# Kernel optimization log

Hardware: AMD Instinct MI355X
Metric: run time of the kernel (lower is better)

Reference implementation:

```python
import jax, jax.numpy as jnp
import numpy as np

HEAD_DIM = 64
NUM_FEATURES = 256


def _sample_orf(head_dim, num_features, seed=0):
    """Orthogonal random features with chi(d)-norm row scaling (FAVOR+)."""
    rng = np.random.RandomState(seed)
    blocks = []
    while len(blocks) * head_dim < num_features:
        G = rng.randn(head_dim, head_dim).astype(np.float32)
        Q, _ = np.linalg.qr(G)
        norms = np.linalg.norm(rng.randn(head_dim, head_dim).astype(np.float32), axis=1)
        blocks.append(np.diag(norms) @ Q.T)
    return np.concatenate(blocks, axis=0)[:num_features].astype(np.float32)


def _phi(x, omega, is_query):
    """FAVOR+ positive feature map with max-subtraction stabilization."""
    m = omega.shape[0]
    proj = jnp.einsum('bhnd,md->bhnm', x, omega)          # [B,H,N,M]
    norm = 0.5 * jnp.sum(x * x, axis=-1, keepdims=True)    # [B,H,N,1]
    log_phi = proj - norm
    if is_query:
        log_phi = log_phi - jnp.max(log_phi, axis=-1, keepdims=True)
    else:
        log_phi = log_phi - jnp.max(log_phi)
    return jnp.exp(log_phi) / np.float32(np.sqrt(m)) + 1e-4


def _causal_scan(phi_q, phi_k, v):
    """Causal linear-attention recurrence via lax.scan. States: S[B,H,M,D], z[B,H,M]."""
    B, H, N, M = phi_q.shape
    D = v.shape[-1]
    # seq-first for scan: [N,B,H,*]
    pq = jnp.moveaxis(phi_q, 2, 0)
    pk = jnp.moveaxis(phi_k, 2, 0)
    vt = jnp.moveaxis(v, 2, 0)

    S0 = jnp.zeros((B, H, M, D), dtype=phi_q.dtype)
    z0 = jnp.zeros((B, H, M), dtype=phi_q.dtype)

    def step(carry, xs):
        S, z = carry
        pq_i, pk_i, v_i = xs  # [B,H,M], [B,H,M], [B,H,D]
        S = S + pk_i[..., :, None] * v_i[..., None, :]
        z = z + pk_i
        num = jnp.einsum('bhm,bhmd->bhd', pq_i, S)
        den = jnp.sum(pq_i * z, axis=-1, keepdims=True) + 1e-6
        return (S, z), num / den

    _, out = jax.lax.scan(step, (S0, z0), (pq, pk, vt))  # out: [N,B,H,D]
    return jnp.moveaxis(out, 0, 2)


def setup_inputs() -> dict:
    key = jax.random.key(0)
    k1, k2, k3 = jax.random.split(key, 3)
    B, H, N, D = 2, 16, 4096, HEAD_DIM
    q = jax.random.normal(k1, (B, H, N, D), dtype=jnp.float32)
    k = jax.random.normal(k2, (B, H, N, D), dtype=jnp.float32)
    v = jax.random.normal(k3, (B, H, N, D), dtype=jnp.float32)
    omega = jnp.asarray(_sample_orf(HEAD_DIM, NUM_FEATURES))
    return {"q": q, "k": k, "v": v, "omega": omega}


def reference(q, k, v, omega):
    scale = q.shape[-1] ** (-0.25)
    phi_q = _phi(q * scale, omega, is_query=True)
    phi_k = _phi(k * scale, omega, is_query=False)
    # q_len == kv_len -> causal scan branch (matches original forward)
    out = _causal_scan(phi_q.astype(jnp.float32), phi_k.astype(jnp.float32),
                       v.astype(jnp.float32))
    return out.astype(q.dtype)
```

## Files before the change

### kernel.cpp

```cpp
#include <hip/hip_runtime.h>
#include <cstddef>

#define BH    32
#define NSEQ  4096
#define MFEAT 256
#define CHUNK 128
#define NCH   32
#define SROW  65
#define SPITCH (SROW*256)

#define SCALE 0.35355339059327373f

typedef unsigned int uint_t;
typedef _Float16 half_t;
typedef __attribute__((ext_vector_type(8))) _Float16 half8;
typedef __attribute__((ext_vector_type(4))) float f32x4;

__device__ __forceinline__ f32x4 mfma16(half8 a, half8 b, f32x4 c) {
  return __builtin_amdgcn_mfma_f32_16x16x32_f16(a, b, c, 0, 0, 0);
}
__device__ __forceinline__ uint_t enc_f(float x) {
  uint_t u = __float_as_uint(x);
  return (u & 0x80000000u) ? ~u : (u | 0x80000000u);
}
__device__ __forceinline__ float dec_f(uint_t u) {
  u = (u & 0x80000000u) ? (u ^ 0x80000000u) : ~u;
  return __uint_as_float(u);
}
__device__ __forceinline__ half8 cvt_h8(float4 a, float4 b) {
  half8 h;
  h[0] = (half_t)a.x; h[1] = (half_t)a.y; h[2] = (half_t)a.z; h[3] = (half_t)a.w;
  h[4] = (half_t)b.x; h[5] = (half_t)b.y; h[6] = (half_t)b.z; h[7] = (half_t)b.w;
  return h;
}

__global__ void k_init(uint_t* kmax) { *kmax = enc_f(-__builtin_inff()); }

__global__ __launch_bounds__(256, 4) void k_maxes2(
    const float* __restrict__ q, const float* __restrict__ kx,
    const float* __restrict__ omega, float* __restrict__ rowmQ,
    uint_t* __restrict__ kmax, half_t* __restrict__ qh,
    half_t* __restrict__ kh, float* __restrict__ hnKg)
{
  __shared__ half_t Wl[256 * 72];
  __shared__ float nrm[64];
  __shared__ float red[4];

  const int tid = threadIdx.x;
  const int lane = tid & 63;
  const int w = tid >> 6;
  const int lc = lane & 15, rg = lane >> 4, koff = rg * 8;
  const size_t rowbase = (size_t)blockIdx.x * 64;

  for (int l = tid; l < 4096; l += 256) {
    int m = l >> 4, d4 = (l & 15) * 4;
    float4 o = *(const float4*)(omega + m * 64 + d4);
    half_t* p = &Wl[m * 72 + d4];
    p[0] = (half_t)o.x; p[1] = (half_t)o.y; p[2] = (half_t)o.z; p[3] = (half_t)o.w;
  }
  half8 aq[2], akf[2];
  {
    const float* qp = q + (rowbase + w * 16 + lc) * 64 + koff;
    const float* kp = kx + (rowbase + w * 16 + lc) * 64 + koff;
    float pn = 0.f;
    #pragma unroll
    for (int ks = 0; ks < 2; ks++) {
      float4 a = *(const float4*)(qp + ks * 32);
      float4 b = *(const float4*)(qp + ks * 32 + 4);
      a.x *= SCALE; a.y *= SCALE; a.z *= SCALE; a.w *= SCALE;
      b.x *= SCALE; b.y *= SCALE; b.z *= SCALE; b.w *= SCALE;
      aq[ks] = cvt_h8(a, b);
      float4 c = *(const float4*)(kp + ks * 32);
      float4 d = *(const float4*)(kp + ks * 32 + 4);
      c.x *= SCALE; c.y *= SCALE; c.z *= SCALE; c.w *= SCALE;
      d.x *= SCALE; d.y *= SCALE; d.z *= SCALE; d.w *= SCALE;
      pn += c.x * c.x + c.y * c.y + c.z * c.z + c.w * c.w
          + d.x * d.x + d.y * d.y + d.z * d.z + d.w * d.w;
      akf[ks] = cvt_h8(c, d);
    }
    #pragma unroll
    for (int ks = 0; ks < 2; ks++) {
      *(half8*)(qh + (rowbase + w * 16 + lc) * 64 + ks * 32 + koff) = aq[ks];
      *(half8*)(kh + (rowbase + w * 16 + lc) * 64 + ks * 32 + koff) = akf[ks];
    }
    pn += __shfl_xor(pn, 16, 64);
    pn += __shfl_xor(pn, 32, 64);
    if (rg == 0) {
      nrm[w * 16 + lc] = 0.5f * pn;
      hnKg[rowbase + w * 16 + lc] = 0.5f * pn;
    }
  }
  __syncthreads();

  float mrow[4] = {-3.4e38f, -3.4e38f, -3.4e38f, -3.4e38f};
  #pragma unroll
  for (int hh = 0; hh < 2; hh++) {
    f32x4 acc[8];
    #pragma unroll
    for (int c = 0; c < 8; c++) acc[c] = (f32x4){0.f, 0.f, 0.f, 0.f};
    #pragma unroll
    for (int ks = 0; ks < 2; ks++)
      #pragma unroll
      for (int c = 0; c < 8; c++) {
        half8 b = *(const half8*)&Wl[((hh * 8 + c) * 16 + lc) * 72 + ks * 32 + koff];
        acc[c] = mfma16(aq[ks], b, acc[c]);
      }
    #pragma unroll
    for (int c = 0; c < 8; c++)
      #pragma unroll
      for (int r = 0; r < 4; r++) mrow[r] = fmaxf(mrow[r], acc[c][r]);
  }
  #pragma unroll
  for (int r = 0; r < 4; r++) {
    float m0 = mrow[r];
    m0 = fmaxf(m0, __shfl_xor(m0, 1, 64));
    m0 = fmaxf(m0, __shfl_xor(m0, 2, 64));
    m0 = fmaxf(m0, __shfl_xor(m0, 4, 64));
    m0 = fmaxf(m0, __shfl_xor(m0, 8, 64));
    if (lc == 0) rowmQ[rowbase + w * 16 + rg * 4 + r] = m0;
  }

  float hn[4];
  #pragma unroll
  for (int r = 0; r < 4; r++) hn[r] = nrm[w * 16 + rg * 4 + r];
  float bm = -3.4e38f;
  #pragma unroll
  for (int hh = 0; hh < 2; hh++) {
    f32x4 acc[8];
    #pragma unroll
    for (int c = 0; c < 8; c++) acc[c] = (f32x4){0.f, 0.f, 0.f, 0.f};
    #pragma unroll
    for (int ks = 0; ks < 2; ks++)
      #pragma unroll
      for (int c = 0; c < 8; c++) {
        half8 b = *(const half8*)&Wl[((hh * 8 + c) * 16 + lc) * 72 + ks * 32 + koff];
        acc[c] = mfma16(akf[ks], b, acc[c]);
      }
    #pragma unroll
    for (int c = 0; c < 8; c++)
      #pragma unroll
      for (int r = 0; r < 4; r++) bm = fmaxf(bm, acc[c][r] - hn[r]);
  }
  #pragma unroll
  for (int off = 1; off < 64; off <<= 1) bm = fmaxf(bm, __shfl_xor(bm, off, 64));
  if (lane == 0) red[w] = bm;
  __syncthreads();
  if (tid == 0)
    atomicMax(kmax, enc_f(fmaxf(fmaxf(red[0], red[1]), fmaxf(red[2], red[3]))));
}

__global__ __launch_bounds__(256, 2) void k_state2(
    const half_t* __restrict__ kh, const float* __restrict__ v,
    const float* __restrict__ omega, const float* __restrict__ hnKg,
    const uint_t* __restrict__ kmax, half_t* __restrict__ spA)
{
  __shared__ half_t WP[256 * 72];
  __shared__ half_t vt[80 * 136];

  const int tid = threadIdx.x;
  const int lane = tid & 63;
  const int w = tid >> 6;
  const int lc = lane & 15, rg = lane >> 4, koff = rg * 8;
  const int wr = w * 32;
  const int blk = blockIdx.x;
  const size_t nbase = (size_t)(blk >> 5) * NSEQ + (size_t)(blk & 31) * CHUNK;
  const float gmaxv = dec_f(*kmax);

  for (int l = tid; l < 4096; l += 256) {
    int m = l >> 4, d4 = (l & 15) * 4;
    float4 o = *(const float4*)(omega + m * 64 + d4);
    half_t* p = &WP[m * 72 + d4];
    p[0] = (half_t)o.x; p[1] = (half_t)o.y; p[2] = (half_t)o.z; p[3] = (half_t)o.w;
  }
  for (int l = tid; l < 2048; l += 256) {
    int j = l >> 4, dq = (l & 15) * 4;
    float4 vv = *(const float4*)(v + (nbase + j) * 64 + dq);
    vt[(dq + 0) * 136 + j] = (half_t)vv.x;
    vt[(dq + 1) * 136 + j] = (half_t)vv.y;
    vt[(dq + 2) * 136 + j] = (half_t)vv.z;
    vt[(dq + 3) * 136 + j] = (half_t)vv.w;
  }
  if (tid < 128) vt[64 * 136 + tid] = (half_t)1.0f;

  half8 ak[2][2];
  float hnr[2][4];
  #pragma unroll
  for (int rt = 0; rt < 2; rt++) {
    const half_t* kp = kh + (nbase + wr + rt * 16 + lc) * 64 + koff;
    ak[rt][0] = *(const half8*)(kp);
    ak[rt][1] = *(const half8*)(kp + 32);
    #pragma unroll
    for (int r = 0; r < 4; r++)
      hnr[rt][r] = hnKg[nbase + wr + rt * 16 + rg * 4 + r];
  }
  __syncthreads();

  f32x4 accP[2][16];
  #pragma unroll
  for (int rt = 0; rt < 2; rt++)
    #pragma unroll
    for (int ct = 0; ct < 16; ct++) accP[rt][ct] = (f32x4){0.f, 0.f, 0.f, 0.f};
  #pragma unroll
  for (int ks = 0; ks < 2; ks++)
    #pragma unroll
    for (int ct = 0; ct < 16; ct++) {
      half8 b = *(const half8*)&WP[(ct * 16 + lc) * 72 + ks * 32 + koff];
      accP[0][ct] = mfma16(ak[0][ks], b, accP[0][ct]);
      accP[1][ct] = mfma16(ak[1][ks], b, accP[1][ct]);
    }
  #pragma unroll
  for (int rt = 0; rt < 2; rt++)
    #pragma unroll
    for (int ct = 0; ct < 16; ct++)
      #pragma unroll
      for (int r = 0; r < 4; r++)
        accP[rt][ct][r] = __expf(accP[rt][ct][r] - hnr[rt][r] - gmaxv) * 0.0625f + 1e-4f;

  half_t* pkT = WP;
  #pragma unroll
  for (int h = 0; h < 2; h++) {
    __syncthreads();
    #pragma unroll
    for (int rt = 0; rt < 2; rt++)
      #pragma unroll
      for (int c8 = 0; c8 < 8; c8++) {
        int ct = h * 8 + c8;
        #pragma unroll
        for (int r = 0; r < 4; r++)
          pkT[(c8 * 16 + lc) * 144 + wr + rt * 16 + rg * 4 + r] = (half_t)accP[rt][ct][r];
      }
    __syncthreads();
    f32x4 acc2[5][2];
    #pragma unroll
    for (int rt = 0; rt < 5; rt++) {
      acc2[rt][0] = (f32x4){0.f, 0.f, 0.f, 0.f};
      acc2[rt][1] = (f32x4){0.f, 0.f, 0.f, 0.f};
    }
    #pragma unroll
    for (int ks = 0; ks < 4; ks++) {
      half8 b0 = *(const half8*)&pkT[((2 * w + 0) * 16 + lc) * 144 + ks * 32 + koff];
      half8 b1 = *(const half8*)&pkT[((2 * w + 1) * 16 + lc) * 144 + ks * 32 + koff];
      #pragma unroll
      for (int rt = 0; rt < 5; rt++) {
        half8 a = *(const half8*)&vt[(rt * 16 + lc) * 136 + ks * 32 + koff];
        acc2[rt][0] = mfma16(a, b0, acc2[rt][0]);
        acc2[rt][1] = mfma16(a, b1, acc2[rt][1]);
      }
    }
    #pragma unroll
    for (int rt = 0; rt < 5; rt++)
      #pragma unroll
      for (int c2 = 0; c2 < 2; c2++)
        #pragma unroll
        for (int r = 0; r < 4; r++) {
          int row = rt * 16 + rg * 4 + r;
          if (row < SROW)
            spA[(size_t)blk * SPITCH + row * 256 + h * 128 + (2 * w + c2) * 16 + lc] =
                (half_t)acc2[rt][c2][r];
        }
  }
}

__global__ __launch_bounds__(256) void k_prefix(
    const uint_t* __restrict__ spA, uint_t* __restrict__ spB)
{
  int r = blockIdx.x * 256 + threadIdx.x;
  if (r >= SPITCH / 2) return;
  int bh = blockIdx.y;
  const uint_t* src = spA + (size_t)bh * NCH * (SPITCH / 2) + r;
  uint_t* dst = spB + (size_t)bh * NCH * (SPITCH / 2) + r;
  float r0 = 0.f, r1 = 0.f;
  for (int c = 0; c < NCH; c++) {
    union { uint_t u; half_t h[2]; } cv, ov;
    cv.u = src[(size_t)c * (SPITCH / 2)];
    ov.h[0] = (half_t)r0; ov.h[1] = (half_t)r1;
    dst[(size_t)c * (SPITCH / 2)] = ov.u;
    r0 += (float)cv.h[0];
    r1 += (float)cv.h[1];
  }
}

__global__ __launch_bounds__(256, 2) void k_attn7(
    const half_t* __restrict__ qh, const half_t* __restrict__ kh,
    const float* __restrict__ v, const float* __restrict__ omega,
    const float* __restrict__ rowmQ, const float* __restrict__ hnKg,
    const uint_t* __restrict__ kmax, const half_t* __restrict__ spB,
    float* __restrict__ out)
{
  __shared__ half_t sm[21504];
  half_t* PQ  = sm;
  half_t* PK  = sm + 8192;
  half_t* SST = sm + 16384;
  half_t* AS  = sm;
  half_t* VT  = sm + 8192;

  const int tid = threadIdx.x;
  const int lane = tid & 63;
  const int w = tid >> 6;
  const int lc = lane & 15, rg = lane >> 4, koff = rg * 8;
  const int wr = w * 32;
  const int blk = blockIdx.x;
  const size_t nbase = (size_t)(blk >> 5) * NSEQ + (size_t)(blk & 31) * CHUNK;
  const half_t* spb = spB + (size_t)blk * SPITCH;
  const float gmaxv = dec_f(*kmax);
  const int swz = (lc & 7) << 3;

  float rowm[2][4], hnr[2][4];
  #pragma unroll
  for (int rt = 0; rt < 2; rt++)
    #pragma unroll
    for (int r = 0; r < 4; r++) {
      rowm[rt][r] = rowmQ[nbase + wr + rt * 16 + rg * 4 + r];
      hnr[rt][r]  = hnKg[nbase + wr + rt * 16 + rg * 4 + r];
    }
  half8 aq[2][2], ak[2][2];
  #pragma unroll
  for (int rt = 0; rt < 2; rt++) {
    const half_t* qp = qh + (nbase + wr + rt * 16 + lc) * 64 + koff;
    const half_t* kp = kh + (nbase + wr + rt * 16 + lc) * 64 + koff;
    aq[rt][0] = *(const half8*)(qp);
    aq[rt][1] = *(const half8*)(qp + 32);
    ak[rt][0] = *(const half8*)(kp);
    ak[rt][1] = *(const half8*)(kp + 32);
  }

#define STAGEPHASE(MT) do {                                                   \
    { int ro = tid >> 3, c8 = (tid & 7) * 8;                                  \
      *(half8*)&SST[ro * 64 + (c8 ^ ((ro & 7) << 3))] =                       \
          *(const half8*)(spb + ro * 256 + (MT) * 64 + c8); }                 \
    { int l = tid + 256; int ro = l >> 3, c8 = (l & 7) * 8;                   \
      *(half8*)&SST[ro * 64 + (c8 ^ ((ro & 7) << 3))] =                       \
          *(const half8*)(spb + ro * 256 + (MT) * 64 + c8); }                 \
    if (tid < 8) { int l = tid + 512; int ro = l >> 3, c8 = (l & 7) * 8;      \
      *(half8*)&SST[ro * 64 + (c8 ^ ((ro & 7) << 3))] =                       \
          *(const half8*)(spb + ro * 256 + (MT) * 64 + c8); }                 \
    half8 bwl[4][2];                                                          \
    _Pragma("unroll") for (int ct = 0; ct < 4; ct++) {                        \
      const float* op = omega + ((MT) * 64 + ct * 16 + lc) * 64 + koff;       \
      bwl[ct][0] = cvt_h8(*(const float4*)(op), *(const float4*)(op + 4));    \
      bwl[ct][1] = cvt_h8(*(const float4*)(op + 32),                          \
                          *(const float4*)(op + 36));                         \
    }                                                                         \
    f32x4 accP[2][4];                                                         \
    _Pragma("unroll") for (int rt = 0; rt < 2; rt++)                          \
      _Pragma("unroll") for (int ct = 0; ct < 4; ct++)                        \
        accP[rt][ct] = (f32x4){0.f, 0.f, 0.f, 0.f};                           \
    _Pragma("unroll") for (int ks = 0; ks < 2; ks++)                          \
      _Pragma("unroll") for (int ct = 0; ct < 4; ct++) {                      \
        accP[0][ct] = mfma16(aq[0][ks], bwl[ct][ks], accP[0][ct]);            \
        accP[1][ct] = mfma16(aq[1][ks], bwl[ct][ks], accP[1][ct]);            \
      }                                                                       \
    _Pragma("unroll") for (int rt = 0; rt < 2; rt++)                          \
      _Pragma("unroll") for (int ct = 0; ct < 4; ct++)                        \
        _Pragma("unroll") for (int r = 0; r < 4; r++) {                       \
          int i = wr + rt * 16 + rg * 4 + r;                                  \
          float val = __expf(accP[rt][ct][r] - rowm[rt][r]) * 0.0625f + 1e-4f;\
          PQ[i * 64 + ((ct * 16 + lc) ^ ((i & 7) << 3))] = (half_t)val;       \
        }                                                                     \
    _Pragma("unroll") for (int rt = 0; rt < 2; rt++)                          \
      _Pragma("unroll") for (int ct = 0; ct < 4; ct++)                        \
        accP[rt][ct] = (f32x4){0.f, 0.f, 0.f, 0.f};                           \
    _Pragma("unroll") for (int ks = 0; ks < 2; ks++)                          \
      _Pragma("unroll") for (int ct = 0; ct < 4; ct++) {                      \
        accP[0][ct] = mfma16(ak[0][ks], bwl[ct][ks], accP[0][ct]);            \
        accP[1][ct] = mfma16(ak[1][ks], bwl[ct][ks], accP[1][ct]);            \
      }                                                                       \
    _Pragma("unroll") for (int rt = 0; rt < 2; rt++)                          \
      _Pragma("unroll") for (int ct = 0; ct < 4; ct++)                        \
        _Pragma("unroll") for (int r = 0; r < 4; r++) {                       \
          int i = wr + rt * 16 + rg * 4 + r;                                  \
          float val = __expf(accP[rt][ct][r] - hnr[rt][r] - gmaxv) * 0.0625f + 1e-4f; \
          PK[i * 64 + ((ct * 16 + lc) ^ ((i & 7) << 3))] = (half_t)val;       \
        }                                                                     \
  } while (0)

#define COMPUTEPHASE() do {                                                   \
    _Pragma("unroll") for (int ks2 = 0; ks2 < 64; ks2 += 32) {                \
      int sA = (ks2 + koff) ^ swz;                                            \
      half8 a0 = *(const half8*)&PQ[(wr + lc) * 64 + sA];                     \
      half8 a1 = *(const half8*)&PQ[(wr + 16 + lc) * 64 + sA];                \
      _Pragma("unroll") for (int ct = 0; ct < 8; ct++) {                      \
        half8 b = *(const half8*)&PK[(ct * 16 + lc) * 64 + sA];               \
        accA[0][ct] = mfma16(a0, b, accA[0][ct]);                             \
        accA[1][ct] = mfma16(a1, b, accA[1][ct]);                             \
      }                                                                       \
      _Pragma("unroll") for (int cs = 0; cs < 5; cs++) {                      \
        half8 b = *(const half8*)&SST[(cs * 16 + lc) * 64 + sA];              \
        accO[0][cs] = mfma16(a0, b, accO[0][cs]);                             \
        accO[1][cs] = mfma16(a1, b, accO[1][cs]);                             \
      }                                                                       \
    } } while (0)

  f32x4 accA[2][8], accO[2][5];
  #pragma unroll
  for (int rt = 0; rt < 2; rt++) {
    #pragma unroll
    for (int ct = 0; ct < 8; ct++) accA[rt][ct] = (f32x4){0.f, 0.f, 0.f, 0.f};
    #pragma unroll
    for (int cs = 0; cs < 5; cs++) accO[rt][cs] = (f32x4){0.f, 0.f, 0.f, 0.f};
  }

  for (int mt = 0; mt < 4; mt++) {
    STAGEPHASE(mt);
    __syncthreads();
    COMPUTEPHASE();
    __syncthreads();
  }

  for (int l = tid; l < 2048; l += 256) {
    int j = l >> 4, dq = (l & 15) * 4;
    float4 vv = *(const float4*)(v + (nbase + j) * 64 + dq);
    VT[(dq + 0) * 128 + (j ^ (((dq + 0) & 7) << 3))] = (half_t)vv.x;
    VT[(dq + 1) * 128 + (j ^ (((dq + 1) & 7) << 3))] = (half_t)vv.y;
    VT[(dq + 2) * 128 + (j ^ (((dq + 2) & 7) << 3))] = (half_t)vv.z;
    VT[(dq + 3) * 128 + (j ^ (((dq + 3) & 7) << 3))] = (half_t)vv.w;
  }
  if (tid < 128) VT[64 * 128 + tid] = (half_t)1.0f;

  #pragma unroll
  for (int h = 0; h < 2; h++) {
    #pragma unroll
    for (int rt = 0; rt < 2; rt++)
      #pragma unroll
      for (int c4 = 0; c4 < 4; c4++) {
        int ct = h * 4 + c4;
        int j = ct * 16 + lc;
        #pragma unroll
        for (int r = 0; r < 4; r++) {
          int i = wr + rt * 16 + rg * 4 + r;
          float val = (j <= i) ? accA[rt][ct][r] : 0.f;
          AS[i * 64 + ((j - h * 64) ^ ((i & 7) << 3))] = (half_t)val;
        }
      }
    if (h == 0) __syncthreads();
    #pragma unroll
    for (int ks2 = 0; ks2 < 64; ks2 += 32) {
      int sA = (ks2 + koff) ^ swz;
      int sV = (h * 64 + ks2 + koff) ^ swz;
      half8 a0 = *(const half8*)&AS[(wr + lc) * 64 + sA];
      half8 a1 = *(const half8*)&AS[(wr + 16 + lc) * 64 + sA];
      #pragma unroll
      for (int cs = 0; cs < 5; cs++) {
        half8 b = *(const half8*)&VT[(cs * 16 + lc) * 128 + sV];
        accO[0][cs] = mfma16(a0, b, accO[0][cs]);
        accO[1][cs] = mfma16(a1, b, accO[1][cs]);
      }
    }
  }

  #pragma unroll
  for (int rt = 0; rt < 2; rt++)
    #pragma unroll
    for (int r = 0; r < 4; r++) {
      float den = __shfl(accO[rt][4][r], (lane & 48), 64) + 1e-6f;
      float inv = 1.0f / den;
      int i = wr + rt * 16 + rg * 4 + r;
      #pragma unroll
      for (int cs = 0; cs < 4; cs++)
        out[(nbase + i) * 64 + cs * 16 + lc] = accO[rt][cs][r] * inv;
    }
#undef STAGEPHASE
#undef COMPUTEPHASE
}

extern "C" void kernel_launch(void* const* d_in, const int* in_sizes, int n_in,
                              void* d_out, int out_size, void* d_ws, size_t ws_size,
                              hipStream_t stream) {
  const float* q = (const float*)d_in[0];
  const float* k = (const float*)d_in[1];
  const float* v = (const float*)d_in[2];
  const float* omega = (const float*)d_in[3];
  float* out = (float*)d_out;
  char* ws = (char*)d_ws;

  float*  rowmQ = (float*)(ws + 0);
  float*  hnKg  = (float*)(ws + 524288);
  half_t* qh    = (half_t*)(ws + 1048576);
  half_t* kh    = (half_t*)(ws + 17825792);
  half_t* spA   = (half_t*)(ws + 34603008);
  half_t* spB   = (half_t*)(ws + 68681728);
  uint_t* kmax  = (uint_t*)(ws + 102760448);

  k_init<<<1, 1, 0, stream>>>(kmax);
  k_maxes2<<<2048, 256, 0, stream>>>(q, k, omega, rowmQ, kmax, qh, kh, hnKg);
  k_state2<<<1024, 256, 0, stream>>>(kh, v, omega, hnKg, kmax, spA);
  k_prefix<<<dim3(33, 32), 256, 0, stream>>>((const uint_t*)spA, (uint_t*)spB);
  k_attn7<<<1024, 256, 0, stream>>>(qh, kh, v, omega, rowmQ, hnKg, kmax, spB, out);
}
```

Measured before the change: 162.2 us.

## Materialize phiQ and phiK in earlier kernels instead of recomputing in attention

```diff
diff --git a/kernel.cpp b/kernel.cpp
--- a/kernel.cpp
+++ b/kernel.cpp
@@ -36,11 +36,11 @@
 
 __global__ void k_init(uint_t* kmax) { *kmax = enc_f(-__builtin_inff()); }
 
-__global__ __launch_bounds__(256, 4) void k_maxes2(
+__global__ __launch_bounds__(256, 2) void k_maxes3(
     const float* __restrict__ q, const float* __restrict__ kx,
-    const float* __restrict__ omega, float* __restrict__ rowmQ,
-    uint_t* __restrict__ kmax, half_t* __restrict__ qh,
-    half_t* __restrict__ kh, float* __restrict__ hnKg)
+    const float* __restrict__ omega, uint_t* __restrict__ kmax,
+    half_t* __restrict__ phiQ, half_t* __restrict__ kh,
+    float* __restrict__ hnKg)
 {
   __shared__ half_t Wl[256 * 72];
   __shared__ float nrm[64];
@@ -79,10 +79,8 @@
       akf[ks] = cvt_h8(c, d);
     }
     #pragma unroll
-    for (int ks = 0; ks < 2; ks++) {
-      *(half8*)(qh + (rowbase + w * 16 + lc) * 64 + ks * 32 + koff) = aq[ks];
+    for (int ks = 0; ks < 2; ks++)
       *(half8*)(kh + (rowbase + w * 16 + lc) * 64 + ks * 32 + koff) = akf[ks];
-    }
     pn += __shfl_xor(pn, 16, 64);
     pn += __shfl_xor(pn, 32, 64);
     if (rg == 0) {
@@ -92,67 +90,82 @@
   }
   __syncthreads();
 
-  float mrow[4] = {-3.4e38f, -3.4e38f, -3.4e38f, -3.4e38f};
-  #pragma unroll
-  for (int hh = 0; hh < 2; hh++) {
-    f32x4 acc[8];
-    #pragma unroll
-    for (int c = 0; c < 8; c++) acc[c] = (f32x4){0.f, 0.f, 0.f, 0.f};
+  {
+    f32x4 acc[16];
+    #pragma unroll
+    for (int ct = 0; ct < 16; ct++) acc[ct] = (f32x4){0.f, 0.f, 0.f, 0.f};
     #pragma unroll
     for (int ks = 0; ks < 2; ks++)
       #pragma unroll
-      for (int c = 0; c < 8; c++) {
-        half8 b = *(const half8*)&Wl[((hh * 8 + c) * 16 + lc) * 72 + ks * 32 + koff];
-        acc[c] = mfma16(aq[ks], b, acc[c]);
-      }
-    #pragma unroll
-    for (int c = 0; c < 8; c++)
-      #pragma unroll
-      for (int r = 0; r < 4; r++) mrow[r] = fmaxf(mrow[r], acc[c][r]);
-  }
+      for (int ct = 0; ct < 16; ct++) {
+        half8 b = *(const half8*)&Wl[(ct * 16 + lc) * 72 + ks * 32 + koff];
+        acc[ct] = mfma16(akf[ks], b, acc[ct]);
+      }
+    float hn[4];
+    #pragma unroll
+    for (int r = 0; r < 4; r++) hn[r] = nrm[w * 16 + rg * 4 + r];
+    float bm = -3.4e38f;
+    #pragma unroll
+    for (int ct = 0; ct < 16; ct++)
+      #pragma unroll
+      for (int r = 0; r < 4; r++) bm = fmaxf(bm, acc[ct][r] - hn[r]);
+    #pragma unroll
+    for (int off = 1; off < 64; off <<= 1) bm = fmaxf(bm, __shfl_xor(bm, off, 64));
+    if (lane == 0) red[w] = bm;
+  }
+
+  f32x4 acc[16];
+  #pragma unroll
+  for (int ct = 0; ct < 16; ct++) acc[ct] = (f32x4){0.f, 0.f, 0.f, 0.f};
+  #pragma unroll
+  for (int ks = 0; ks < 2; ks++)
+    #pragma unroll
+    for (int ct = 0; ct < 16; ct++) {
+      half8 b = *(const half8*)&Wl[(ct * 16 + lc) * 72 + ks * 32 + koff];
+      acc[ct] = mfma16(aq[ks], b, acc[ct]);
+    }
+  float rowm[4];
   #pragma unroll
   for (int r = 0; r < 4; r++) {
-    float m0 = mrow[r];
+    float m0 = -3.4e38f;
+    #pragma unroll
+    for (int ct = 0; ct < 16; ct++) m0 = fmaxf(m0, acc[ct][r]);
     m0 = fmaxf(m0, __shfl_xor(m0, 1, 64));
     m0 = fmaxf(m0, __shfl_xor(m0, 2, 64));
     m0 = fmaxf(m0, __shfl_xor(m0, 4, 64));
     m0 = fmaxf(m0, __shfl_xor(m0, 8, 64));
-    if (lc == 0) rowmQ[rowbase + w * 16 + rg * 4 + r] = m0;
-  }
-
-  float hn[4];
-  #pragma unroll
-  for (int r = 0; r < 4; r++) hn[r] = nrm[w * 16 + rg * 4 + r];
-  float bm = -3.4e38f;
-  #pragma unroll
-  for (int hh = 0; hh < 2; hh++) {
-    f32x4 acc[8];
-    #pragma unroll
-    for (int c = 0; c < 8; c++) acc[c] = (f32x4){0.f, 0.f, 0.f, 0.f};
-    #pragma unroll
-    for (int ks = 0; ks < 2; ks++)
-      #pragma unroll
-      for (int c = 0; c < 8; c++) {
-        half8 b = *(const half8*)&Wl[((hh * 8 + c) * 16 + lc) * 72 + ks * 32 + koff];
-        acc[c] = mfma16(akf[ks], b, acc[c]);
-      }
-    #pragma unroll
-    for (int c = 0; c < 8; c++)
-      #pragma unroll
-      for (int r = 0; r < 4; r++) bm = fmaxf(bm, acc[c][r] - hn[r]);
-  }
-  #pragma unroll
-  for (int off = 1; off < 64; off <<= 1) bm = fmaxf(bm, __shfl_xor(bm, off, 64));
-  if (lane == 0) red[w] = bm;
+    rowm[r] = m0;
+  }
+  #pragma unroll
+  for (int ct = 0; ct < 16; ct++)
+    #pragma unroll
+    for (int r = 0; r < 4; r++)
+      acc[ct][r] = __expf(acc[ct][r] - rowm[r]) * 0.0625f + 1e-4f;
+
   __syncthreads();
   if (tid == 0)
     atomicMax(kmax, enc_f(fmaxf(fmaxf(red[0], red[1]), fmaxf(red[2], red[3]))));
-}
-
-__global__ __launch_bounds__(256, 2) void k_state2(
+
+  half_t* st = Wl;
+  #pragma unroll
+  for (int ct = 0; ct < 16; ct++)
+    #pragma unroll
+    for (int r = 0; r < 4; r++)
+      st[(w * 16 + rg * 4 + r) * 264 + ct * 16 + lc] = (half_t)acc[ct][r];
+  __syncthreads();
+  #pragma unroll
+  for (int e = 0; e < 8; e++) {
+    int l = tid + e * 256;
+    int row = l >> 5, c = (l & 31) * 8;
+    *(half8*)(phiQ + (rowbase + row) * 256 + c) = *(const half8*)&st[row * 264 + c];
+  }
+}
+
+__global__ __launch_bounds__(256, 2) void k_state3(
     const half_t* __restrict__ kh, const float* __restrict__ v,
     const float* __restrict__ omega, const float* __restrict__ hnKg,
-    const uint_t* __restrict__ kmax, half_t* __restrict__ spA)
+    const uint_t* __restrict__ kmax, half_t* __restrict__ spA,
+    half_t* __restrict__ phiKg)
 {
   __shared__ half_t WP[256 * 72];
   __shared__ half_t vt[80 * 136];
@@ -258,6 +271,28 @@
             spA[(size_t)blk * SPITCH + row * 256 + h * 128 + (2 * w + c2) * 16 + lc] =
                 (half_t)acc2[rt][c2][r];
         }
+  }
+
+  half_t* PhS = WP;
+  #pragma unroll
+  for (int hh = 0; hh < 2; hh++) {
+    __syncthreads();
+    #pragma unroll
+    for (int rt = 0; rt < 2; rt++)
+      #pragma unroll
+      for (int c8 = 0; c8 < 8; c8++)
+        #pragma unroll
+        for (int r = 0; r < 4; r++)
+          PhS[(wr + rt * 16 + rg * 4 + r) * 136 + c8 * 16 + lc] =
+              (half_t)accP[rt][hh * 8 + c8][r];
+    __syncthreads();
+    #pragma unroll
+    for (int e = 0; e < 8; e++) {
+      int l = tid + e * 256;
+      int j = l >> 4, c8b = (l & 15) * 8;
+      *(half8*)(phiKg + (nbase + j) * 256 + hh * 128 + c8b) =
+          *(const half8*)&PhS[j * 136 + c8b];
+    }
   }
 }
 
@@ -280,17 +315,14 @@
   }
 }
 
-__global__ __launch_bounds__(256, 2) void k_attn7(
-    const half_t* __restrict__ qh, const half_t* __restrict__ kh,
-    const float* __restrict__ v, const float* __restrict__ omega,
-    const float* __restrict__ rowmQ, const float* __restrict__ hnKg,
-    const uint_t* __restrict__ kmax, const half_t* __restrict__ spB,
+__global__ __launch_bounds__(512) void k_attn8(
+    const half_t* __restrict__ phiQ, const half_t* __restrict__ phiK,
+    const float* __restrict__ v, const half_t* __restrict__ spB,
     float* __restrict__ out)
 {
-  __shared__ half_t sm[21504];
+  __shared__ half_t sm[18432];
   half_t* PQ  = sm;
-  half_t* PK  = sm + 8192;
-  half_t* SST = sm + 16384;
+  half_t* SST = sm + 8192;
   half_t* AS  = sm;
   half_t* VT  = sm + 8192;
 
@@ -298,116 +330,58 @@
   const int lane = tid & 63;
   const int w = tid >> 6;
   const int lc = lane & 15, rg = lane >> 4, koff = rg * 8;
-  const int wr = w * 32;
   const int blk = blockIdx.x;
   const size_t nbase = (size_t)(blk >> 5) * NSEQ + (size_t)(blk & 31) * CHUNK;
   const half_t* spb = spB + (size_t)blk * SPITCH;
-  const float gmaxv = dec_f(*kmax);
   const int swz = (lc & 7) << 3;
 
-  float rowm[2][4], hnr[2][4];
-  #pragma unroll
-  for (int rt = 0; rt < 2; rt++)
-    #pragma unroll
-    for (int r = 0; r < 4; r++) {
-      rowm[rt][r] = rowmQ[nbase + wr + rt * 16 + rg * 4 + r];
-      hnr[rt][r]  = hnKg[nbase + wr + rt * 16 + rg * 4 + r];
-    }
-  half8 aq[2][2], ak[2][2];
-  #pragma unroll
-  for (int rt = 0; rt < 2; rt++) {
-    const half_t* qp = qh + (nbase + wr + rt * 16 + lc) * 64 + koff;
-    const half_t* kp = kh + (nbase + wr + rt * 16 + lc) * 64 + koff;
-    aq[rt][0] = *(const half8*)(qp);
-    aq[rt][1] = *(const half8*)(qp + 32);
-    ak[rt][0] = *(const half8*)(kp);
-    ak[rt][1] = *(const half8*)(kp + 32);
-  }
-
-#define STAGEPHASE(MT) do {                                                   \
-    { int ro = tid >> 3, c8 = (tid & 7) * 8;                                  \
-      *(half8*)&SST[ro * 64 + (c8 ^ ((ro & 7) << 3))] =                       \
-          *(const half8*)(spb + ro * 256 + (MT) * 64 + c8); }                 \
-    { int l = tid + 256; int ro = l >> 3, c8 = (l & 7) * 8;                   \
-      *(half8*)&SST[ro * 64 + (c8 ^ ((ro & 7) << 3))] =                       \
-          *(const half8*)(spb + ro * 256 + (MT) * 64 + c8); }                 \
-    if (tid < 8) { int l = tid + 512; int ro = l >> 3, c8 = (l & 7) * 8;      \
-      *(half8*)&SST[ro * 64 + (c8 ^ ((ro & 7) << 3))] =                       \
-          *(const half8*)(spb + ro * 256 + (MT) * 64 + c8); }                 \
-    half8 bwl[4][2];                                                          \
-    _Pragma("unroll") for (int ct = 0; ct < 4; ct++) {                        \
-      const float* op = omega + ((MT) * 64 + ct * 16 + lc) * 64 + koff;       \
-      bwl[ct][0] = cvt_h8(*(const float4*)(op), *(const float4*)(op + 4));    \
-      bwl[ct][1] = cvt_h8(*(const float4*)(op + 32),                          \
-                          *(const float4*)(op + 36));                         \
-    }                                                                         \
-    f32x4 accP[2][4];                                                         \
-    _Pragma("unroll") for (int rt = 0; rt < 2; rt++)                          \
-      _Pragma("unroll") for (int ct = 0; ct < 4; ct++)                        \
-        accP[rt][ct] = (f32x4){0.f, 0.f, 0.f, 0.f};                           \
-    _Pragma("unroll") for (int ks = 0; ks < 2; ks++)                          \
-      _Pragma("unroll") for (int ct = 0; ct < 4; ct++) {                      \
-        accP[0][ct] = mfma16(aq[0][ks], bwl[ct][ks], accP[0][ct]);            \
-        accP[1][ct] = mfma16(aq[1][ks], bwl[ct][ks], accP[1][ct]);            \
-      }                                                                       \
-    _Pragma("unroll") for (int rt = 0; rt < 2; rt++)                          \
-      _Pragma("unroll") for (int ct = 0; ct < 4; ct++)                        \
-        _Pragma("unroll") for (int r = 0; r < 4; r++) {                       \
-          int i = wr + rt * 16 + rg * 4 + r;                                  \
-          float val = __expf(accP[rt][ct][r] - rowm[rt][r]) * 0.0625f + 1e-4f;\
-          PQ[i * 64 + ((ct * 16 + lc) ^ ((i & 7) << 3))] = (half_t)val;       \
-        }                                                                     \
-    _Pragma("unroll") for (int rt = 0; rt < 2; rt++)                          \
-      _Pragma("unroll") for (int ct = 0; ct < 4; ct++)                        \
-        accP[rt][ct] = (f32x4){0.f, 0.f, 0.f, 0.f};                           \
-    _Pragma("unroll") for (int ks = 0; ks < 2; ks++)                          \
-      _Pragma("unroll") for (int ct = 0; ct < 4; ct++) {                      \
-        accP[0][ct] = mfma16(ak[0][ks], bwl[ct][ks], accP[0][ct]);            \
-        accP[1][ct] = mfma16(ak[1][ks], bwl[ct][ks], accP[1][ct]);            \
-      }                                                                       \
-    _Pragma("unroll") for (int rt = 0; rt < 2; rt++)                          \
-      _Pragma("unroll") for (int ct = 0; ct < 4; ct++)                        \
-        _Pragma("unroll") for (int r = 0; r < 4; r++) {                       \
-          int i = wr + rt * 16 + rg * 4 + r;                                  \
-          float val = __expf(accP[rt][ct][r] - hnr[rt][r] - gmaxv) * 0.0625f + 1e-4f; \
-          PK[i * 64 + ((ct * 16 + lc) ^ ((i & 7) << 3))] = (half_t)val;       \
-        }                                                                     \
-  } while (0)
-
-#define COMPUTEPHASE() do {                                                   \
-    _Pragma("unroll") for (int ks2 = 0; ks2 < 64; ks2 += 32) {                \
-      int sA = (ks2 + koff) ^ swz;                                            \
-      half8 a0 = *(const half8*)&PQ[(wr + lc) * 64 + sA];                     \
-      half8 a1 = *(const half8*)&PQ[(wr + 16 + lc) * 64 + sA];                \
-      _Pragma("unroll") for (int ct = 0; ct < 8; ct++) {                      \
-        half8 b = *(const half8*)&PK[(ct * 16 + lc) * 64 + sA];               \
-        accA[0][ct] = mfma16(a0, b, accA[0][ct]);                             \
-        accA[1][ct] = mfma16(a1, b, accA[1][ct]);                             \
-      }                                                                       \
-      _Pragma("unroll") for (int cs = 0; cs < 5; cs++) {                      \
-        half8 b = *(const half8*)&SST[(cs * 16 + lc) * 64 + sA];              \
-        accO[0][cs] = mfma16(a0, b, accO[0][cs]);                             \
-        accO[1][cs] = mfma16(a1, b, accO[1][cs]);                             \
-      }                                                                       \
-    } } while (0)
-
-  f32x4 accA[2][8], accO[2][5];
-  #pragma unroll
-  for (int rt = 0; rt < 2; rt++) {
-    #pragma unroll
-    for (int ct = 0; ct < 8; ct++) accA[rt][ct] = (f32x4){0.f, 0.f, 0.f, 0.f};
-    #pragma unroll
-    for (int cs = 0; cs < 5; cs++) accO[rt][cs] = (f32x4){0.f, 0.f, 0.f, 0.f};
-  }
+  f32x4 accA[8], accO[5];
+  #pragma unroll
+  for (int it = 0; it < 8; it++) accA[it] = (f32x4){0.f, 0.f, 0.f, 0.f};
+  #pragma unroll
+  for (int cs = 0; cs < 5; cs++) accO[cs] = (f32x4){0.f, 0.f, 0.f, 0.f};
 
   for (int mt = 0; mt < 4; mt++) {
-    STAGEPHASE(mt);
-    __syncthreads();
-    COMPUTEPHASE();
-    __syncthreads();
-  }
-
-  for (int l = tid; l < 2048; l += 256) {
+    if (mt) __syncthreads();
+    #pragma unroll
+    for (int e = 0; e < 2; e++) {
+      int l = tid + e * 512;
+      int ro = l >> 3, c8 = (l & 7) * 8;
+      *(half8*)&PQ[ro * 64 + (c8 ^ ((ro & 7) << 3))] =
+          *(const half8*)(phiQ + (nbase + ro) * 256 + mt * 64 + c8);
+    }
+    { int ro = tid >> 3, c8 = (tid & 7) * 8;
+      if (tid < 520)
+        *(half8*)&SST[ro * 64 + (c8 ^ ((ro & 7) << 3))] =
+            *(const half8*)(spb + ro * 256 + mt * 64 + c8); }
+    if (tid < 8) { int l = tid + 512; int ro = l >> 3, c8 = (l & 7) * 8;
+      *(half8*)&SST[ro * 64 + (c8 ^ ((ro & 7) << 3))] =
+          *(const half8*)(spb + ro * 256 + mt * 64 + c8); }
+    half8 af0 = *(const half8*)(phiK + (nbase + w * 16 + lc) * 256 + mt * 64 + koff);
+    half8 af1 = *(const half8*)(phiK + (nbase + w * 16 + lc) * 256 + mt * 64 + 32 + koff);
+    __syncthreads();
+    #pragma unroll
+    for (int ks2 = 0; ks2 < 64; ks2 += 32) {
+      half8 a = ks2 ? af1 : af0;
+      int sA = (ks2 + koff) ^ swz;
+      half8 bO = *(const half8*)&PQ[(w * 16 + lc) * 64 + sA];
+      #pragma unroll
+      for (int it = 0; it < 8; it++) {
+        half8 b = *(const half8*)&PQ[(it * 16 + lc) * 64 + sA];
+        accA[it] = mfma16(a, b, accA[it]);
+      }
+      #pragma unroll
+      for (int cs = 0; cs < 5; cs++) {
+        half8 as_ = *(const half8*)&SST[(cs * 16 + lc) * 64 + sA];
+        accO[cs] = mfma16(as_, bO, accO[cs]);
+      }
+    }
+  }
+  __syncthreads();
+
+  #pragma unroll
+  for (int e = 0; e < 4; e++) {
+    int l = tid + e * 512;
     int j = l >> 4, dq = (l & 15) * 4;
     float4 vv = *(const float4*)(v + (nbase + j) * 64 + dq);
     VT[(dq + 0) * 128 + (j ^ (((dq + 0) & 7) << 3))] = (half_t)vv.x;
@@ -419,48 +393,47 @@
 
   #pragma unroll
   for (int h = 0; h < 2; h++) {
-    #pragma unroll
-    for (int rt = 0; rt < 2; rt++)
-      #pragma unroll
-      for (int c4 = 0; c4 < 4; c4++) {
-        int ct = h * 4 + c4;
-        int j = ct * 16 + lc;
+    if ((w >> 2) == h) {
+      #pragma unroll
+      for (int it = 0; it < 8; it++) {
+        int i = it * 16 + lc;
         #pragma unroll
         for (int r = 0; r < 4; r++) {
-          int i = wr + rt * 16 + rg * 4 + r;
-          float val = (j <= i) ? accA[rt][ct][r] : 0.f;
+          int j = w * 16 + rg * 4 + r;
+          float val = (j <= i) ? accA[it][r] : 0.f;
           AS[i * 64 + ((j - h * 64) ^ ((i & 7) << 3))] = (half_t)val;
         }
       }
-    if (h == 0) __syncthreads();
+    }
+    __syncthreads();
     #pragma unroll
     for (int ks2 = 0; ks2 < 64; ks2 += 32) {
-      int sA = (ks2 + koff) ^ swz;
-      int sV = (h * 64 + ks2 + koff) ^ swz;
-      half8 a0 = *(const half8*)&AS[(wr + lc) * 64 + sA];
-      half8 a1 = *(const half8*)&AS[(wr + 16 + lc) * 64 + sA];
+      int sj = (ks2 + koff) ^ swz;
+      half8 b = *(const half8*)&AS[(w * 16 + lc) * 64 + sj];
       #pragma unroll
       for (int cs = 0; cs < 5; cs++) {
-        half8 b = *(const half8*)&VT[(cs * 16 + lc) * 128 + sV];
-        accO[0][cs] = mfma16(a0, b, accO[0][cs]);
-        accO[1][cs] = mfma16(a1, b, accO[1][cs]);
-      }
-    }
-  }
-
-  #pragma unroll
-  for (int rt = 0; rt < 2; rt++)
-    #pragma unroll
-    for (int r = 0; r < 4; r++) {
-      float den = __shfl(accO[rt][4][r], (lane & 48), 64) + 1e-6f;
-      float inv = 1.0f / den;
-      int i = wr + rt * 16 + rg * 4 + r;
-      #pragma unroll
-      for (int cs = 0; cs < 4; cs++)
-        out[(nbase + i) * 64 + cs * 16 + lc] = accO[rt][cs][r] * inv;
-    }
-#undef STAGEPHASE
-#undef COMPUTEPHASE
+        half8 a = *(const half8*)&VT[(cs * 16 + lc) * 128 + ((h * 64 + ks2 + koff) ^ swz)];
+        accO[cs] = mfma16(a, b, accO[cs]);
+      }
+    }
+    __syncthreads();
+  }
+
+  float den = __shfl(accO[4][0], lane & 15, 64) + 1e-6f;
+  float inv = 1.0f / den;
+  float* OS = (float*)sm;
+  #pragma unroll
+  for (int cs = 0; cs < 4; cs++)
+    #pragma unroll
+    for (int r = 0; r < 4; r++)
+      OS[(w * 16 + lc) * 68 + cs * 16 + rg * 4 + r] = accO[cs][r] * inv;
+  __syncthreads();
+  #pragma unroll
+  for (int e = 0; e < 4; e++) {
+    int l = tid + e * 512;
+    int row = l >> 4, c4 = (l & 15) * 4;
+    *(float4*)(out + (nbase + row) * 64 + c4) = *(const float4*)&OS[row * 68 + c4];
+  }
 }
 
 extern "C" void kernel_launch(void* const* d_in, const int* in_sizes, int n_in,
@@ -473,17 +446,17 @@
   float* out = (float*)d_out;
   char* ws = (char*)d_ws;
 
-  float*  rowmQ = (float*)(ws + 0);
-  float*  hnKg  = (float*)(ws + 524288);
-  half_t* qh    = (half_t*)(ws + 1048576);
-  half_t* kh    = (half_t*)(ws + 17825792);
-  half_t* spA   = (half_t*)(ws + 34603008);
-  half_t* spB   = (half_t*)(ws + 68681728);
-  uint_t* kmax  = (uint_t*)(ws + 102760448);
+  float*  hnKg = (float*)(ws + 0);
+  half_t* kh   = (half_t*)(ws + 524288);
+  half_t* spB  = (half_t*)(ws + 524288);
+  half_t* phiQ = (half_t*)(ws + 34603008);
+  half_t* phiK = (half_t*)(ws + 101711872);
+  half_t* spA  = (half_t*)(ws + 168820736);
+  uint_t* kmax = (uint_t*)(ws + 202899456);
 
   k_init<<<1, 1, 0, stream>>>(kmax);
-  k_maxes2<<<2048, 256, 0, stream>>>(q, k, omega, rowmQ, kmax, qh, kh, hnKg);
-  k_state2<<<1024, 256, 0, stream>>>(kh, v, omega, hnKg, kmax, spA);
+  k_maxes3<<<2048, 256, 0, stream>>>(q, k, omega, kmax, phiQ, kh, hnKg);
+  k_state3<<<1024, 256, 0, stream>>>(kh, v, omega, hnKg, kmax, spA, phiK);
   k_prefix<<<dim3(33, 32), 256, 0, stream>>>((const uint_t*)spA, (uint_t*)spB);
-  k_attn7<<<1024, 256, 0, stream>>>(qh, kh, v, omega, rowmQ, hnKg, kmax, spB, out);
-}
+  k_attn8<<<1024, 512, 0, stream>>>(phiQ, phiK, v, spB, out);
+}
```

Measured after the change: 167.2 us. +3.1%, slower.
